# Optimization experiments

Measured on AMD Instinct MI355X. Metric: run time of the kernel, lower is better.

Reference implementation:

```python
import jax, jax.numpy as jnp
import numpy as np
import math

HEADS = 8
HIDDEN = 512
HEAD_DIM = HIDDEN // HEADS
BATCH = 16
N = 512
ALPHA = 1.0 / math.sqrt(HEAD_DIM)


def setup_inputs() -> dict:
    key = jax.random.key(0)
    ks = jax.random.split(key, 6)
    stdv_qkv = 1.0 / math.sqrt(HEAD_DIM)
    stdv_o = 1.0 / math.sqrt(HIDDEN)
    return {
        "x": jax.random.normal(ks[0], (BATCH, N, HIDDEN), dtype=jnp.float32),
        "edge": jax.random.normal(ks[1], (HEADS, BATCH, N, N), dtype=jnp.float32),
        "Wq": jax.random.uniform(ks[2], (HEADS, HIDDEN, HEAD_DIM), jnp.float32, -stdv_qkv, stdv_qkv),
        "Wk": jax.random.uniform(ks[3], (HEADS, HIDDEN, HEAD_DIM), jnp.float32, -stdv_qkv, stdv_qkv),
        "Wv": jax.random.uniform(ks[4], (HEADS, HIDDEN, HEAD_DIM), jnp.float32, -stdv_qkv, stdv_qkv),
        "Wo": jax.random.uniform(ks[5], (HIDDEN, HIDDEN), jnp.float32, -stdv_o, stdv_o),
    }


def reference(x, edge, Wq, Wk, Wv, Wo):
    # per-head projections: x [b,n,h] x W [g,h,d] -> [g,b,n,d]
    Q = jnp.einsum("bnh,ghd->gbnd", x, Wq)
    K = jnp.einsum("bnh,ghd->gbnd", x, Wk)
    V = jnp.einsum("bnh,ghd->gbnd", x, Wv)
    # edge-biased attention scores [g,b,n,n]
    S = edge + ALPHA * jnp.einsum("gbnd,gbmd->gbnm", Q, K)
    S = jax.nn.softmax(S, axis=-1)
    # attend and merge heads: [g,b,n,d] -> [b,n,g*d]
    o = jnp.einsum("gbnm,gbmd->bngd", S, V)
    o = o.reshape(o.shape[0], o.shape[1], -1)
    return o @ Wo
```

## Files before the change

### kernel.cpp

```cpp
#include <hip/hip_runtime.h>

typedef __bf16 bf16;
typedef __bf16 bf16x4 __attribute__((ext_vector_type(4)));
typedef __bf16 bf16x8 __attribute__((ext_vector_type(8)));
typedef float f32x4 __attribute__((ext_vector_type(4)));

#define ALPHA_ 0.125f


__device__ __forceinline__ void gload16(const void* g, void* l) {
  __builtin_amdgcn_global_load_lds((__attribute__((address_space(1))) void*)(g),
                                   (__attribute__((address_space(3))) void*)(l),
                                   16, 0, 0);
}

__global__ void cast_x_kernel(const float* __restrict__ x, bf16* __restrict__ xb) {
  int i = blockIdx.x * 256 + threadIdx.x;
  float4 v = ((const float4*)x)[i];
  bf16x4 o = {(bf16)v.x, (bf16)v.y, (bf16)v.z, (bf16)v.w};
  ((bf16x4*)xb)[i] = o;
}

__global__ void prep_w_kernel(const float* __restrict__ Wq, const float* __restrict__ Wk,
                              const float* __restrict__ Wv, bf16* __restrict__ wcat) {
  int i = blockIdx.x * 256 + threadIdx.x;
  int h = i & 511, j = i >> 9;
  int qkv = j >> 9, g = (j >> 6) & 7, d = j & 63;
  const float* W = (qkv == 0) ? Wq : ((qkv == 1) ? Wk : Wv);
  wcat[i] = (bf16)W[((g << 9) + h) * 64 + d];
}

__global__ void prep_wo_kernel(const float* __restrict__ Wo, bf16* __restrict__ wot) {
  int i = blockIdx.x * 256 + threadIdx.x;
  int k = i & 511, n = i >> 9;
  wot[i] = (bf16)Wo[(k << 9) + n];
}

template <int MODE>
__global__ __launch_bounds__(256, 2) void gemm_bt_kernel(
    const bf16* __restrict__ A, const bf16* __restrict__ Bt, int Kdim, int Ndim,
    float* __restrict__ Cf, bf16* __restrict__ Qo, bf16* __restrict__ Ko,
    bf16* __restrict__ Vto) {
  __shared__ bf16 lA[128 * 32];
  __shared__ bf16 lB[128 * 32];
  const int t = threadIdx.x;
  const int w = t >> 6;
  const int lane = t & 63;
  const int lhi = lane >> 4, llo = lane & 15;
  const int m0 = blockIdx.y * 128, n0 = blockIdx.x * 128;
  const int wr = (w >> 1) * 64, wc = (w & 1) * 64;

  f32x4 acc[4][4] = {};
  const int nkt = Kdim >> 5;
  for (int kt = 0; kt < nkt; ++kt) {
#pragma unroll
    for (int c = 0; c < 2; ++c) {
      int u = c * 256 + t;
      const bf16* ga = A + (size_t)(m0 + (u >> 2)) * Kdim + kt * 32 + (u & 3) * 8;
      gload16(ga, &lA[c * 2048 + w * 512]);
      const bf16* gb = Bt + (size_t)(n0 + (u >> 2)) * Kdim + kt * 32 + (u & 3) * 8;
      gload16(gb, &lB[c * 2048 + w * 512]);
    }
    __syncthreads();
    bf16x8 af[4], bfr[4];
#pragma unroll
    for (int i = 0; i < 4; ++i) {
      af[i] = *(const bf16x8*)&lA[(wr + i * 16 + llo) * 32 + lhi * 8];
      bfr[i] = *(const bf16x8*)&lB[(wc + i * 16 + llo) * 32 + lhi * 8];
    }
#pragma unroll
    for (int i = 0; i < 4; ++i)
#pragma unroll
      for (int j = 0; j < 4; ++j)
        acc[i][j] = __builtin_amdgcn_mfma_f32_16x16x32_bf16(af[i], bfr[j], acc[i][j], 0, 0, 0);
    __syncthreads();
  }

#pragma unroll
  for (int i = 0; i < 4; ++i) {
    int row = m0 + wr + i * 16 + lhi * 4;
#pragma unroll
    for (int j = 0; j < 4; ++j) {
      int col = n0 + wc + j * 16 + llo;
#pragma unroll
      for (int r = 0; r < 4; ++r) {
        float v = acc[i][j][r];
        int rr = row + r;
        if (MODE == 0) {
          int qkv = col >> 9, g = (col >> 6) & 7, d = col & 63;
          bf16 bv = (bf16)v;
          if (qkv == 0)
            Qo[((size_t)g * 8192 + rr) * 64 + d] = bv;
          else if (qkv == 1)
            Ko[((size_t)g * 8192 + rr) * 64 + d] = bv;
          else {
            int b = rr >> 9, n = rr & 511;
            Vto[(((size_t)g * 16 + b) * 64 + d) * 512 + n] = bv;
          }
        } else {
          Cf[(size_t)rr * Ndim + col] = v;
        }
      }
    }
  }
}

__global__ __launch_bounds__(256, 2) void attn_kernel(
    const bf16* __restrict__ Qa, const bf16* __restrict__ Ka,
    const bf16* __restrict__ Vta, const float* __restrict__ edge,
    bf16* __restrict__ Oatt) {
  __shared__ bf16 lK[128 * 64];
  __shared__ bf16 lV[64 * 128];
  __shared__ bf16 lP[4][32 * 128];
  const int t = threadIdx.x, w = t >> 6, lane = t & 63;
  const int lhi = lane >> 4, llo = lane & 15;
  const int qt = blockIdx.x, b = blockIdx.y, g = blockIdx.z;
  const int q0 = qt * 128 + w * 32;
  const bf16* Qg = Qa + ((size_t)g * 8192 + b * 512) * 64;
  const bf16* Kg = Ka + ((size_t)g * 8192 + b * 512) * 64;
  const bf16* Vg = Vta + ((size_t)g * 16 + b) * (64 * 512);
  const float* eg = edge + ((size_t)g * 16 + b) * (512 * 512);

  bf16x8 qf[2][2];
#pragma unroll
  for (int mi = 0; mi < 2; ++mi)
#pragma unroll
    for (int ks = 0; ks < 2; ++ks)
      qf[mi][ks] = *(const bf16x8*)(Qg + (size_t)(q0 + mi * 16 + llo) * 64 + ks * 32 + lhi * 8);

  f32x4 oacc[2][4] = {};
  float mrow[2] = {-1e30f, -1e30f};
  float lrow[2] = {0.f, 0.f};

  for (int kv0 = 0; kv0 < 512; kv0 += 128) {
#pragma unroll
    for (int c = 0; c < 4; ++c) {
      int u = c * 256 + t;
      int kr = u >> 3, kc = (u & 7) * 8;
      bf16x8 kvv = *(const bf16x8*)(Kg + (size_t)(kv0 + kr) * 64 + kc);
      *(bf16x8*)&lK[(kr * 64 + kc) ^ ((kr & 7) << 3)] = kvv;
      int vr = u >> 4, vc = (u & 15) * 8;
      bf16x8 vv = *(const bf16x8*)(Vg + (size_t)vr * 512 + kv0 + vc);
      *(bf16x8*)&lV[(vr * 128 + vc) ^ ((vr & 7) << 3)] = vv;
    }
    f32x4 ef[2][8];
#pragma unroll
    for (int mi = 0; mi < 2; ++mi)
#pragma unroll
      for (int ni = 0; ni < 8; ++ni)
        ef[mi][ni] = *(const f32x4*)(eg + (size_t)(q0 + mi * 16 + llo) * 512 + kv0 + ni * 16 + lhi * 4);
    __syncthreads();

    f32x4 sc[2][8] = {};
#pragma unroll
    for (int ks = 0; ks < 2; ++ks) {
      bf16x8 kf[8];
#pragma unroll
      for (int ni = 0; ni < 8; ++ni) {
        int row = ni * 16 + llo;
        kf[ni] = *(const bf16x8*)&lK[(row * 64 + ks * 32 + lhi * 8) ^ ((row & 7) << 3)];
      }
#pragma unroll
      for (int mi = 0; mi < 2; ++mi)
#pragma unroll
        for (int ni = 0; ni < 8; ++ni)
          sc[mi][ni] = __builtin_amdgcn_mfma_f32_16x16x32_bf16(kf[ni], qf[mi][ks], sc[mi][ni], 0, 0, 0);
    }

    float sscale[2];
#pragma unroll
    for (int mi = 0; mi < 2; ++mi) {
      float mx = -1e30f;
#pragma unroll
      for (int ni = 0; ni < 8; ++ni)
#pragma unroll
        for (int r = 0; r < 4; ++r) {
          float sv = fmaf(ALPHA_, sc[mi][ni][r], ef[mi][ni][r]);
          sc[mi][ni][r] = sv;
          mx = fmaxf(mx, sv);
        }
      mx = fmaxf(mx, __shfl_xor(mx, 16));
      mx = fmaxf(mx, __shfl_xor(mx, 32));
      float mnew = fmaxf(mrow[mi], mx);
      float s = __expf(mrow[mi] - mnew);
      mrow[mi] = mnew;
      sscale[mi] = s;
      float rsum = 0.f;
#pragma unroll
      for (int ni = 0; ni < 8; ++ni)
#pragma unroll
        for (int r = 0; r < 4; ++r) {
          float p = __expf(sc[mi][ni][r] - mnew);
          sc[mi][ni][r] = p;
          rsum += p;
        }
      rsum += __shfl_xor(rsum, 16);
      rsum += __shfl_xor(rsum, 32);
      lrow[mi] = lrow[mi] * s + rsum;
    }

#pragma unroll
    for (int mi = 0; mi < 2; ++mi) {
#pragma unroll
      for (int r = 0; r < 4; ++r) {
        float sq = __shfl(sscale[mi], (lane & 48) | (lhi * 4 + r));
#pragma unroll
        for (int nc = 0; nc < 4; ++nc) oacc[mi][nc][r] *= sq;
      }
    }

    bf16* Pw = lP[w];
#pragma unroll
    for (int mi = 0; mi < 2; ++mi)
#pragma unroll
      for (int ni = 0; ni < 8; ++ni) {
        int row = mi * 16 + llo;
        int colb = ni * 16 + lhi * 4;
        bf16x4 pv = {(bf16)sc[mi][ni][0], (bf16)sc[mi][ni][1],
                     (bf16)sc[mi][ni][2], (bf16)sc[mi][ni][3]};
        *(bf16x4*)&Pw[(row * 128 + colb) ^ ((row & 7) << 3)] = pv;
      }

#pragma unroll
    for (int ks2 = 0; ks2 < 4; ++ks2) {
      bf16x8 pf[2], vf[4];
#pragma unroll
      for (int mi = 0; mi < 2; ++mi) {
        int row = mi * 16 + llo;
        pf[mi] = *(const bf16x8*)&Pw[(row * 128 + ks2 * 32 + lhi * 8) ^ ((row & 7) << 3)];
      }
#pragma unroll
      for (int nc = 0; nc < 4; ++nc) {
        int row = nc * 16 + llo;
        vf[nc] = *(const bf16x8*)&lV[(row * 128 + ks2 * 32 + lhi * 8) ^ ((row & 7) << 3)];
      }
#pragma unroll
      for (int mi = 0; mi < 2; ++mi)
#pragma unroll
        for (int nc = 0; nc < 4; ++nc)
          oacc[mi][nc] = __builtin_amdgcn_mfma_f32_16x16x32_bf16(pf[mi], vf[nc], oacc[mi][nc], 0, 0, 0);
    }
    __syncthreads();
  }

#pragma unroll
  for (int mi = 0; mi < 2; ++mi) {
    float rcpl = 1.0f / lrow[mi];
#pragma unroll
    for (int r = 0; r < 4; ++r) {
      float lr = __shfl(rcpl, (lane & 48) | (lhi * 4 + r));
      int qrow = q0 + mi * 16 + lhi * 4 + r;
#pragma unroll
      for (int nc = 0; nc < 4; ++nc) {
        float ov = oacc[mi][nc][r] * lr;
        Oatt[((size_t)b * 512 + qrow) * 512 + g * 64 + nc * 16 + llo] = (bf16)ov;
      }
    }
  }
}

extern "C" void kernel_launch(void* const* d_in, const int* in_sizes, int n_in,
                              void* d_out, int out_size, void* d_ws, size_t ws_size,
                              hipStream_t stream) {
  (void)in_sizes; (void)n_in; (void)out_size; (void)ws_size;
  const float* x = (const float*)d_in[0];
  const float* edge = (const float*)d_in[1];
  const float* Wq = (const float*)d_in[2];
  const float* Wk = (const float*)d_in[3];
  const float* Wv = (const float*)d_in[4];
  const float* Wo = (const float*)d_in[5];
  float* out = (float*)d_out;

  char* ws = (char*)d_ws;
  bf16* xb   = (bf16*)(ws + 0);
  bf16* wcat = (bf16*)(ws + 8388608);
  bf16* wot  = (bf16*)(ws + 9961472);
  bf16* Qa   = (bf16*)(ws + 10485760);
  bf16* Ka   = (bf16*)(ws + 18874368);
  bf16* Vta  = (bf16*)(ws + 27262976);
  bf16* Oatt = (bf16*)(ws + 35651584);

  cast_x_kernel<<<4096, 256, 0, stream>>>(x, xb);
  prep_w_kernel<<<3072, 256, 0, stream>>>(Wq, Wk, Wv, wcat);
  prep_wo_kernel<<<1024, 256, 0, stream>>>(Wo, wot);

  gemm_bt_kernel<0><<<dim3(12, 64), 256, 0, stream>>>(xb, wcat, 512, 1536,
                                                      nullptr, Qa, Ka, Vta);
  attn_kernel<<<dim3(4, 16, 8), 256, 0, stream>>>(Qa, Ka, Vta, edge, Oatt);
  gemm_bt_kernel<1><<<dim3(4, 64), 256, 0, stream>>>(Oatt, wot, 512, 512,
                                                     out, nullptr, nullptr, nullptr);
}
```

Before: 116.5 us.

## Restructure attention: smaller tiles, register prefetch of K/V, in-register P via permlane

Shrinks the attention tile to 64 queries by 64 keys per block with 16 rows per wave, doubles the grid, and raises the launch bound to 4 blocks per CU. K/V tiles for the next step are loaded into registers while the current step is computed, which overlaps global loads with compute. The softmax probabilities are packed to bf16 and rearranged with permlane swaps instead of going through shared memory, removing the P staging buffer and its LDS traffic. Costs are twice as many barriers per row of keys and less reuse of each K/V tile, since it is now shared by fewer query rows.

```diff
diff --git a/kernel.cpp b/kernel.cpp
--- a/kernel.cpp
+++ b/kernel.cpp
@@ -105,156 +105,155 @@
   }
 }
 
-__global__ __launch_bounds__(256, 2) void attn_kernel(
+__global__ __launch_bounds__(256, 4) void attn_kernel(
     const bf16* __restrict__ Qa, const bf16* __restrict__ Ka,
     const bf16* __restrict__ Vta, const float* __restrict__ edge,
     bf16* __restrict__ Oatt) {
-  __shared__ bf16 lK[128 * 64];
-  __shared__ bf16 lV[64 * 128];
-  __shared__ bf16 lP[4][32 * 128];
+  __shared__ bf16 lK[64 * 64];
+  __shared__ bf16 lV[64 * 64];
   const int t = threadIdx.x, w = t >> 6, lane = t & 63;
   const int lhi = lane >> 4, llo = lane & 15;
   const int qt = blockIdx.x, b = blockIdx.y, g = blockIdx.z;
-  const int q0 = qt * 128 + w * 32;
+  const int q0 = qt * 64 + w * 16;
   const bf16* Qg = Qa + ((size_t)g * 8192 + b * 512) * 64;
   const bf16* Kg = Ka + ((size_t)g * 8192 + b * 512) * 64;
   const bf16* Vg = Vta + ((size_t)g * 16 + b) * (64 * 512);
   const float* eg = edge + ((size_t)g * 16 + b) * (512 * 512);
 
-  bf16x8 qf[2][2];
-#pragma unroll
-  for (int mi = 0; mi < 2; ++mi)
-#pragma unroll
-    for (int ks = 0; ks < 2; ++ks)
-      qf[mi][ks] = *(const bf16x8*)(Qg + (size_t)(q0 + mi * 16 + llo) * 64 + ks * 32 + lhi * 8);
-
-  f32x4 oacc[2][4] = {};
-  float mrow[2] = {-1e30f, -1e30f};
-  float lrow[2] = {0.f, 0.f};
-
-  for (int kv0 = 0; kv0 < 512; kv0 += 128) {
-#pragma unroll
-    for (int c = 0; c < 4; ++c) {
-      int u = c * 256 + t;
-      int kr = u >> 3, kc = (u & 7) * 8;
-      bf16x8 kvv = *(const bf16x8*)(Kg + (size_t)(kv0 + kr) * 64 + kc);
-      *(bf16x8*)&lK[(kr * 64 + kc) ^ ((kr & 7) << 3)] = kvv;
-      int vr = u >> 4, vc = (u & 15) * 8;
-      bf16x8 vv = *(const bf16x8*)(Vg + (size_t)vr * 512 + kv0 + vc);
-      *(bf16x8*)&lV[(vr * 128 + vc) ^ ((vr & 7) << 3)] = vv;
-    }
-    f32x4 ef[2][8];
-#pragma unroll
-    for (int mi = 0; mi < 2; ++mi)
-#pragma unroll
-      for (int ni = 0; ni < 8; ++ni)
-        ef[mi][ni] = *(const f32x4*)(eg + (size_t)(q0 + mi * 16 + llo) * 512 + kv0 + ni * 16 + lhi * 4);
-    __syncthreads();
-
-    f32x4 sc[2][8] = {};
+  bf16x8 qf[2];
+#pragma unroll
+  for (int ks = 0; ks < 2; ++ks)
+    qf[ks] = *(const bf16x8*)(Qg + (size_t)(q0 + llo) * 64 + ks * 32 + lhi * 8);
+
+  f32x4 oacc[4] = {};
+  float mrow = -3e38f, lrow = 0.f;
+
+  const int r0c = t >> 3, c0c = (t & 7) * 8;
+  const int r1c = (256 + t) >> 3, c1c = c0c;
+
+  bf16x8 kcur[2], vcur[2], knxt[2], vnxt[2];
+  kcur[0] = *(const bf16x8*)(Kg + (size_t)r0c * 64 + c0c);
+  kcur[1] = *(const bf16x8*)(Kg + (size_t)r1c * 64 + c1c);
+  vcur[0] = *(const bf16x8*)(Vg + (size_t)r0c * 512 + c0c);
+  vcur[1] = *(const bf16x8*)(Vg + (size_t)r1c * 512 + c1c);
+
+  for (int it = 0; it < 8; ++it) {
+    const int kv0 = it * 64;
+    *(bf16x8*)&lK[(r0c * 64 + c0c) ^ ((r0c & 7) << 3)] = kcur[0];
+    *(bf16x8*)&lK[(r1c * 64 + c1c) ^ ((r1c & 7) << 3)] = kcur[1];
+    *(bf16x8*)&lV[(r0c * 64 + c0c) ^ ((r0c & 7) << 3)] = vcur[0];
+    *(bf16x8*)&lV[(r1c * 64 + c1c) ^ ((r1c & 7) << 3)] = vcur[1];
+    if (it < 7) {
+      const int kvn = kv0 + 64;
+      knxt[0] = *(const bf16x8*)(Kg + (size_t)(kvn + r0c) * 64 + c0c);
+      knxt[1] = *(const bf16x8*)(Kg + (size_t)(kvn + r1c) * 64 + c1c);
+      vnxt[0] = *(const bf16x8*)(Vg + (size_t)r0c * 512 + kvn + c0c);
+      vnxt[1] = *(const bf16x8*)(Vg + (size_t)r1c * 512 + kvn + c1c);
+    }
+    f32x4 ef[4];
+#pragma unroll
+    for (int ni = 0; ni < 4; ++ni)
+      ef[ni] = *(const f32x4*)(eg + (size_t)(q0 + llo) * 512 + kv0 + ni * 16 + lhi * 4);
+
+    asm volatile("s_waitcnt lgkmcnt(0)" ::: "memory");
+    __builtin_amdgcn_sched_barrier(0);
+    __builtin_amdgcn_s_barrier();
+    __builtin_amdgcn_sched_barrier(0);
+
+    f32x4 sc[4] = {};
 #pragma unroll
     for (int ks = 0; ks < 2; ++ks) {
-      bf16x8 kf[8];
-#pragma unroll
-      for (int ni = 0; ni < 8; ++ni) {
+      bf16x8 kf[4];
+#pragma unroll
+      for (int ni = 0; ni < 4; ++ni) {
         int row = ni * 16 + llo;
         kf[ni] = *(const bf16x8*)&lK[(row * 64 + ks * 32 + lhi * 8) ^ ((row & 7) << 3)];
       }
 #pragma unroll
-      for (int mi = 0; mi < 2; ++mi)
-#pragma unroll
-        for (int ni = 0; ni < 8; ++ni)
-          sc[mi][ni] = __builtin_amdgcn_mfma_f32_16x16x32_bf16(kf[ni], qf[mi][ks], sc[mi][ni], 0, 0, 0);
-    }
-
-    float sscale[2];
-#pragma unroll
-    for (int mi = 0; mi < 2; ++mi) {
-      float mx = -1e30f;
-#pragma unroll
-      for (int ni = 0; ni < 8; ++ni)
-#pragma unroll
-        for (int r = 0; r < 4; ++r) {
-          float sv = fmaf(ALPHA_, sc[mi][ni][r], ef[mi][ni][r]);
-          sc[mi][ni][r] = sv;
-          mx = fmaxf(mx, sv);
-        }
-      mx = fmaxf(mx, __shfl_xor(mx, 16));
-      mx = fmaxf(mx, __shfl_xor(mx, 32));
-      float mnew = fmaxf(mrow[mi], mx);
-      float s = __expf(mrow[mi] - mnew);
-      mrow[mi] = mnew;
-      sscale[mi] = s;
-      float rsum = 0.f;
-#pragma unroll
-      for (int ni = 0; ni < 8; ++ni)
-#pragma unroll
-        for (int r = 0; r < 4; ++r) {
-          float p = __expf(sc[mi][ni][r] - mnew);
-          sc[mi][ni][r] = p;
-          rsum += p;
-        }
-      rsum += __shfl_xor(rsum, 16);
-      rsum += __shfl_xor(rsum, 32);
-      lrow[mi] = lrow[mi] * s + rsum;
-    }
-
-#pragma unroll
-    for (int mi = 0; mi < 2; ++mi) {
+      for (int ni = 0; ni < 4; ++ni)
+        sc[ni] = __builtin_amdgcn_mfma_f32_16x16x32_bf16(kf[ni], qf[ks], sc[ni], 0, 0, 0);
+    }
+
+    float mx = -3e38f;
+#pragma unroll
+    for (int ni = 0; ni < 4; ++ni)
 #pragma unroll
       for (int r = 0; r < 4; ++r) {
-        float sq = __shfl(sscale[mi], (lane & 48) | (lhi * 4 + r));
-#pragma unroll
-        for (int nc = 0; nc < 4; ++nc) oacc[mi][nc][r] *= sq;
-      }
-    }
-
-    bf16* Pw = lP[w];
-#pragma unroll
-    for (int mi = 0; mi < 2; ++mi)
-#pragma unroll
-      for (int ni = 0; ni < 8; ++ni) {
-        int row = mi * 16 + llo;
-        int colb = ni * 16 + lhi * 4;
-        bf16x4 pv = {(bf16)sc[mi][ni][0], (bf16)sc[mi][ni][1],
-                     (bf16)sc[mi][ni][2], (bf16)sc[mi][ni][3]};
-        *(bf16x4*)&Pw[(row * 128 + colb) ^ ((row & 7) << 3)] = pv;
-      }
-
-#pragma unroll
-    for (int ks2 = 0; ks2 < 4; ++ks2) {
-      bf16x8 pf[2], vf[4];
-#pragma unroll
-      for (int mi = 0; mi < 2; ++mi) {
-        int row = mi * 16 + llo;
-        pf[mi] = *(const bf16x8*)&Pw[(row * 128 + ks2 * 32 + lhi * 8) ^ ((row & 7) << 3)];
-      }
+        float sv = fmaf(ALPHA_, sc[ni][r], ef[ni][r]);
+        sc[ni][r] = sv;
+        mx = fmaxf(mx, sv);
+      }
+    mx = fmaxf(mx, __shfl_xor(mx, 16));
+    mx = fmaxf(mx, __shfl_xor(mx, 32));
+    float mnew = fmaxf(mrow, mx);
+    float s = __expf(mrow - mnew);
+    mrow = mnew;
+    float rsum = 0.f;
+#pragma unroll
+    for (int ni = 0; ni < 4; ++ni)
+#pragma unroll
+      for (int r = 0; r < 4; ++r) {
+        float p = __expf(sc[ni][r] - mnew);
+        sc[ni][r] = p;
+        rsum += p;
+      }
+    rsum += __shfl_xor(rsum, 16);
+    rsum += __shfl_xor(rsum, 32);
+    lrow = lrow * s + rsum;
+
+#pragma unroll
+    for (int r = 0; r < 4; ++r) {
+      float sq = __shfl(s, (lane & 48) | (lhi * 4 + r));
+#pragma unroll
+      for (int nc = 0; nc < 4; ++nc) oacc[nc][r] *= sq;
+    }
+
+#pragma unroll
+    for (int ks2 = 0; ks2 < 2; ++ks2) {
+      const int n0 = ks2 * 2, n1 = n0 + 1;
+      unsigned xa, xb, ya, yb;
+      asm("v_cvt_pk_bf16_f32 %0, %1, %2" : "=v"(xa) : "v"(sc[n0][0]), "v"(sc[n0][1]));
+      asm("v_cvt_pk_bf16_f32 %0, %1, %2" : "=v"(xb) : "v"(sc[n0][2]), "v"(sc[n0][3]));
+      asm("v_cvt_pk_bf16_f32 %0, %1, %2" : "=v"(ya) : "v"(sc[n1][0]), "v"(sc[n1][1]));
+      asm("v_cvt_pk_bf16_f32 %0, %1, %2" : "=v"(yb) : "v"(sc[n1][2]), "v"(sc[n1][3]));
+      asm("v_permlane32_swap_b32 %0, %1" : "+v"(xa), "+v"(ya));
+      asm("v_permlane16_swap_b32 %0, %1" : "+v"(xa), "+v"(ya));
+      asm("v_permlane32_swap_b32 %0, %1" : "+v"(xb), "+v"(yb));
+      asm("v_permlane16_swap_b32 %0, %1" : "+v"(xb), "+v"(yb));
+      union { unsigned wd[4]; bf16x8 v; } fu;
+      fu.wd[0] = xa; fu.wd[1] = xb; fu.wd[2] = ya; fu.wd[3] = yb;
+      bf16x8 pf = fu.v;
+
+      bf16x8 vf[4];
 #pragma unroll
       for (int nc = 0; nc < 4; ++nc) {
         int row = nc * 16 + llo;
-        vf[nc] = *(const bf16x8*)&lV[(row * 128 + ks2 * 32 + lhi * 8) ^ ((row & 7) << 3)];
-      }
-#pragma unroll
-      for (int mi = 0; mi < 2; ++mi)
-#pragma unroll
-        for (int nc = 0; nc < 4; ++nc)
-          oacc[mi][nc] = __builtin_amdgcn_mfma_f32_16x16x32_bf16(pf[mi], vf[nc], oacc[mi][nc], 0, 0, 0);
-    }
-    __syncthreads();
-  }
-
-#pragma unroll
-  for (int mi = 0; mi < 2; ++mi) {
-    float rcpl = 1.0f / lrow[mi];
-#pragma unroll
-    for (int r = 0; r < 4; ++r) {
-      float lr = __shfl(rcpl, (lane & 48) | (lhi * 4 + r));
-      int qrow = q0 + mi * 16 + lhi * 4 + r;
-#pragma unroll
-      for (int nc = 0; nc < 4; ++nc) {
-        float ov = oacc[mi][nc][r] * lr;
-        Oatt[((size_t)b * 512 + qrow) * 512 + g * 64 + nc * 16 + llo] = (bf16)ov;
-      }
+        vf[nc] = *(const bf16x8*)&lV[(row * 64 + ks2 * 32 + lhi * 8) ^ ((row & 7) << 3)];
+      }
+#pragma unroll
+      for (int nc = 0; nc < 4; ++nc)
+        oacc[nc] = __builtin_amdgcn_mfma_f32_16x16x32_bf16(pf, vf[nc], oacc[nc], 0, 0, 0);
+    }
+
+    __builtin_amdgcn_sched_barrier(0);
+    __builtin_amdgcn_s_barrier();
+    __builtin_amdgcn_sched_barrier(0);
+
+    if (it < 7) {
+      kcur[0] = knxt[0]; kcur[1] = knxt[1];
+      vcur[0] = vnxt[0]; vcur[1] = vnxt[1];
+    }
+  }
+
+  float rcpl = 1.0f / lrow;
+#pragma unroll
+  for (int r = 0; r < 4; ++r) {
+    float lr = __shfl(rcpl, (lane & 48) | (lhi * 4 + r));
+    int qrow = q0 + lhi * 4 + r;
+#pragma unroll
+    for (int nc = 0; nc < 4; ++nc) {
+      float ov = oacc[nc][r] * lr;
+      Oatt[((size_t)b * 512 + qrow) * 512 + g * 64 + nc * 16 + llo] = (bf16)ov;
     }
   }
 }
@@ -286,7 +285,7 @@
 
   gemm_bt_kernel<0><<<dim3(12, 64), 256, 0, stream>>>(xb, wcat, 512, 1536,
                                                       nullptr, Qa, Ka, Vta);
-  attn_kernel<<<dim3(4, 16, 8), 256, 0, stream>>>(Qa, Ka, Vta, edge, Oatt);
+  attn_kernel<<<dim3(8, 16, 8), 256, 0, stream>>>(Qa, Ka, Vta, edge, Oatt);
   gemm_bt_kernel<1><<<dim3(4, 64), 256, 0, stream>>>(Oatt, wot, 512, 512,
                                                      out, nullptr, nullptr, nullptr);
 }
```

Result: faster. 108.1 us (-7.1%).
